# Kernel tuning notes

Measured on AMD Instinct MI355X. Metric: run time of the kernel, lower is better.

The kernel has to match this reference:

```python
import jax, jax.numpy as jnp
import numpy as np

HIDDEN = 256
HEADS = 8
HEAD_SIZE = HIDDEN // HEADS  # 32
CTX = 512
FF = 4 * HIDDEN
LN_EPS = 1e-5


def setup_inputs() -> dict:
    key = jax.random.key(0)
    ks = jax.random.split(key, 12)
    s = 0.02
    return {
        "x": jax.random.normal(ks[0], (32, CTX, HIDDEN), dtype=jnp.float32),
        # per-head Q/K/V projections, stored [H, D, E] ([in, out] orientation)
        "wq": jax.random.normal(ks[1], (HEADS, HIDDEN, HEAD_SIZE), dtype=jnp.float32) * s,
        "wk": jax.random.normal(ks[2], (HEADS, HIDDEN, HEAD_SIZE), dtype=jnp.float32) * s,
        "wv": jax.random.normal(ks[3], (HEADS, HIDDEN, HEAD_SIZE), dtype=jnp.float32) * s,
        "w_proj": jax.random.normal(ks[4], (HIDDEN, HIDDEN), dtype=jnp.float32) * s,
        "w1": jax.random.normal(ks[5], (HIDDEN, FF), dtype=jnp.float32) * s,
        "b1": jnp.zeros((FF,), dtype=jnp.float32),
        "w2": jax.random.normal(ks[6], (FF, HIDDEN), dtype=jnp.float32) * s,
        "b2": jnp.zeros((HIDDEN,), dtype=jnp.float32),
        "g_ln1": jnp.ones((HIDDEN,), dtype=jnp.float32),
        "be_ln1": jnp.zeros((HIDDEN,), dtype=jnp.float32),
        "g_ln2": jnp.ones((HIDDEN,), dtype=jnp.float32),
        "be_ln2": jnp.zeros((HIDDEN,), dtype=jnp.float32),
    }


def _layernorm(x, g, b):
    mu = jnp.mean(x, axis=-1, keepdims=True)
    var = jnp.var(x, axis=-1, keepdims=True)
    return (x - mu) * jax.lax.rsqrt(var + LN_EPS) * g + b


def reference(x, wq, wk, wv, w_proj, w1, b1, w2, b2, g_ln1, be_ln1, g_ln2, be_ln2):
    B, S, D = x.shape  # S == CTX
    # per-head projections: [B, H, S, E]
    q = jnp.einsum("bsd,hde->bhse", x, wq)
    k = jnp.einsum("bsd,hde->bhse", x, wk)
    v = jnp.einsum("bsd,hde->bhse", x, wv)
    scores = jnp.einsum("bhse,bhte->bhst", q, k) * (HEAD_SIZE ** -0.5)
    causal = jnp.tril(jnp.ones((S, S), dtype=bool))  # [S, S]
    scores = jnp.where(causal, scores, -jnp.inf)
    attn = jax.nn.softmax(scores, axis=-1)
    ctx = jnp.einsum("bhst,bhte->bhse", attn, v)
    ctx = ctx.transpose(0, 2, 1, 3).reshape(B, S, D)  # concat heads
    attn_out = ctx @ w_proj
    h = x + _layernorm(attn_out, g_ln1, be_ln1)
    ff = jax.nn.relu(h @ w1 + b1) @ w2 + b2
    return x + _layernorm(ff, g_ln2, be_ln2)
```

## Files before the change

kernel.cpp:

```cpp
#include <hip/hip_runtime.h>
#include <hip/hip_bf16.h>

#define B_   32
#define S_   512
#define D_   256
#define H_   8
#define E_   32
#define FF_  1024
#define T_   (B_ * S_)

typedef __attribute__((ext_vector_type(8))) short short8;
typedef __attribute__((ext_vector_type(4))) float f32x4;

static __device__ __forceinline__ unsigned short f2bf(float f) {
    union { float f; unsigned int u; } c; c.f = f;
    unsigned int u = c.u;
    u += 0x7fffu + ((u >> 16) & 1u);
    return (unsigned short)(u >> 16);
}
static __device__ __forceinline__ float bf2f(unsigned short u) {
    union { unsigned int u; float f; } c; c.u = ((unsigned int)u) << 16;
    return c.f;
}
static __device__ __forceinline__ unsigned int cvtpk(float lo, float hi) {
    unsigned int r;
    asm("v_cvt_pk_bf16_f32 %0, %1, %2" : "=v"(r) : "v"(lo), "v"(hi));
    return r;
}

#define GLOAD16(g, l) __builtin_amdgcn_global_load_lds( \
    (const __attribute__((address_space(1))) void*)(g), \
    (__attribute__((address_space(3))) void*)(l), 16, 0, 0)

__global__ void prep_kernel(const float* __restrict__ x,
                            const float* __restrict__ wq, const float* __restrict__ wk,
                            const float* __restrict__ wv, const float* __restrict__ w_proj,
                            const float* __restrict__ w1, const float* __restrict__ w2,
                            unsigned short* __restrict__ xb, unsigned short* __restrict__ Wqkv,
                            unsigned short* __restrict__ Wproj, unsigned short* __restrict__ W1t,
                            unsigned short* __restrict__ W2t) {
    int blk = blockIdx.x, tid = threadIdx.x;
    if (blk < 4096) {
        int i = blk * 256 + tid;
        float4 v = *(const float4*)&x[(size_t)i * 4];
        ushort4 o; o.x = f2bf(v.x); o.y = f2bf(v.y); o.z = f2bf(v.z); o.w = f2bf(v.w);
        *(ushort4*)&xb[(size_t)i * 4] = o;
    } else if (blk < 4864) {
        int idx = (blk - 4096) * 256 + tid;
        int nn = idx >> 8, k = idx & 255;
        int which = nn >> 8, r = nn & 255, h = r >> 5, e = r & 31;
        const float* w = (which == 0) ? wq : (which == 1 ? wk : wv);
        float v = w[(h * D_ + k) * E_ + e];
        if (which == 0) v *= 0.17677669529663687f * 1.4426950408889634f;
        Wqkv[idx] = f2bf(v);
    } else if (blk < 5120) {
        int idx = (blk - 4864) * 256 + tid;
        int nn = idx >> 8, k = idx & 255;
        Wproj[idx] = f2bf(w_proj[(size_t)k * 256 + nn]);
    } else if (blk < 6144) {
        int idx = (blk - 5120) * 256 + tid;
        int nn = idx >> 8, k = idx & 255;
        W1t[idx] = f2bf(w1[(size_t)k * 1024 + nn]);
    } else {
        int idx = (blk - 6144) * 256 + tid;
        int nn = idx >> 10, k = idx & 1023;
        W2t[idx] = f2bf(w2[(size_t)k * 256 + nn]);
    }
}

template <int EP, int BN>
__global__ __launch_bounds__(256) void gemm_mfma(const unsigned short* __restrict__ A,
                                                 const unsigned short* __restrict__ Bt,
                                                 const float* __restrict__ bias,
                                                 void* __restrict__ Cout,
                                                 unsigned short* __restrict__ Vout,
                                                 int M, int N, int K) {
    constexpr int FN = BN / 32;
    __shared__ char smem[16384 + BN * 128];
    const int tid = threadIdx.x;
    const int bm = blockIdx.y * 128, bn = blockIdx.x * BN;
    const int wave = tid >> 6, lane = tid & 63;
    const int l15 = lane & 15, kc = lane >> 4;
    const int wr = (wave >> 1) * 64, wc = (wave & 1) * (BN / 2);

    auto stage = [&](int buf, int kt) {
        int k0 = kt * 32;
        char* aBase = smem + buf * 8192;
        char* bBase = smem + 16384 + buf * (BN * 64);
        #pragma unroll
        for (int j = 0; j < 2; ++j) {
            int o = j * 256 + tid;
            int r = o >> 2, c = o & 3;
            int g = c ^ ((r >> 1) & 3);
            GLOAD16(A + (size_t)(bm + r) * K + k0 + g * 8, aBase + o * 16);
        }
        #pragma unroll
        for (int j = 0; j < BN / 64; ++j) {
            int o = j * 256 + tid;
            int r = o >> 2, c = o & 3;
            int g = c ^ ((r >> 1) & 3);
            GLOAD16(Bt + (size_t)(bn + r) * K + k0 + g * 8, bBase + o * 16);
        }
    };

    f32x4 acc[4][FN];
    #pragma unroll
    for (int m = 0; m < 4; ++m)
        #pragma unroll
        for (int n = 0; n < FN; ++n) acc[m][n] = (f32x4){0.f, 0.f, 0.f, 0.f};

    const int NT = K >> 5;
    stage(0, 0);
    __syncthreads();

    int buf = 0;
    for (int kt = 0; kt < NT; ++kt) {
        if (kt + 1 < NT) stage(buf ^ 1, kt + 1);
        const char* aBase = smem + buf * 8192;
        const char* bBase = smem + 16384 + buf * (BN * 64);
        short8 afr[4], bfr[FN];
        #pragma unroll
        for (int m = 0; m < 4; ++m) {
            int row = wr + m * 16 + l15;
            int cc = kc ^ ((row >> 1) & 3);
            afr[m] = *(const short8*)(aBase + row * 64 + cc * 16);
        }
        #pragma unroll
        for (int n = 0; n < FN; ++n) {
            int row = wc + n * 16 + l15;
            int cc = kc ^ ((row >> 1) & 3);
            bfr[n] = *(const short8*)(bBase + row * 64 + cc * 16);
        }
        #pragma unroll
        for (int m = 0; m < 4; ++m)
            #pragma unroll
            for (int n = 0; n < FN; ++n)
                acc[m][n] = __builtin_amdgcn_mfma_f32_16x16x32_bf16(afr[m], bfr[n], acc[m][n], 0, 0, 0);
        __syncthreads();
        buf ^= 1;
    }

    if (EP & 8) {
        #pragma unroll
        for (int n = 0; n < FN; ++n) {
            int col = bn + wc + n * 16 + l15;
            if (col < 512) {
                #pragma unroll
                for (int m = 0; m < 4; ++m) {
                    int row0 = bm + wr + m * 16 + kc * 4;
                    #pragma unroll
                    for (int j = 0; j < 4; ++j)
                        ((unsigned short*)Cout)[(size_t)(row0 + j) * 512 + col] = f2bf(acc[m][n][j]);
                }
            } else {
                int hh = (col - 512) >> 5, e = (col - 512) & 31;
                #pragma unroll
                for (int m = 0; m < 4; ++m) {
                    int row0 = bm + wr + m * 16 + kc * 4;
                    int bb = row0 >> 9, s0 = row0 & 511;
                    ushort4 o4;
                    o4.x = f2bf(acc[m][n][0]); o4.y = f2bf(acc[m][n][1]);
                    o4.z = f2bf(acc[m][n][2]); o4.w = f2bf(acc[m][n][3]);
                    *(ushort4*)&Vout[(size_t)(bb * 8 + hh) * 16384 + e * 512 + s0] = o4;
                }
            }
        }
    } else {
        #pragma unroll
        for (int n = 0; n < FN; ++n) {
            int col = bn + wc + n * 16 + l15;
            float bv = (EP & 1) ? bias[col] : 0.f;
            #pragma unroll
            for (int m = 0; m < 4; ++m) {
                int row0 = bm + wr + m * 16 + kc * 4;
                #pragma unroll
                for (int j = 0; j < 4; ++j) {
                    float v = acc[m][n][j] + bv;
                    if (EP & 2) v = fmaxf(v, 0.f);
                    if (EP & 4) ((unsigned short*)Cout)[(size_t)(row0 + j) * N + col] = f2bf(v);
                    else        ((float*)Cout)[(size_t)(row0 + j) * N + col] = v;
                }
            }
        }
    }
}

__global__ __launch_bounds__(256, 2) void attn_mfma(const unsigned short* __restrict__ qk,
                                                    const unsigned short* __restrict__ vtg,
                                                    unsigned short* __restrict__ ctx) {
    __shared__ unsigned short klds[512 * 32];
    __shared__ unsigned short vlds[32 * 512];
    __shared__ unsigned short plds[4][32 * 64];
    const int blk = blockIdx.x;
    const int bh = blk >> 1, qh = blk & 1;
    const int b = bh >> 3, h = bh & 7;
    const int tid = threadIdx.x;
    const int wave = tid >> 6, lane = tid & 63;
    const int l15 = lane & 15, kc = lane >> 4;

    const unsigned short* kg = qk + (size_t)b * 512 * 512 + 256 + h * 32;
    #pragma unroll
    for (int it = 0; it < 8; ++it) {
        int slot = it * 256 + tid;
        int r = slot >> 2, c = slot & 3;
        GLOAD16(kg + (size_t)r * 512 + (c ^ ((r >> 1) & 3)) * 8, (char*)klds + slot * 16);
    }
    #pragma unroll
    for (int it = 0; it < 8; ++it) {
        int slot = it * 256 + tid;
        int e = slot >> 6, c = slot & 63;
        GLOAD16(vtg + (size_t)bh * 16384 + e * 512 + (c ^ (e & 7)) * 8,
                (char*)vlds + slot * 16);
    }

    const int cA = qh * 4 + wave, cB = 15 - cA;
    short8 qfA[2], qfB[2];
    #pragma unroll
    for (int qm = 0; qm < 2; ++qm) {
        qfA[qm] = *(const short8*)(qk + (size_t)(b * 512 + cA * 32 + qm * 16 + l15) * 512 + h * 32 + kc * 8);
        qfB[qm] = *(const short8*)(qk + (size_t)(b * 512 + cB * 32 + qm * 16 + l15) * 512 + h * 32 + kc * 8);
    }
    __syncthreads();

    unsigned short* pw = plds[wave];
    const int xsw = (l15 & 7) << 1;

    auto process = [&](int cc_, const short8* qf) {
        const int nt = (cc_ >> 1) + 1;
        f32x4 Ofr[2][2];
        float mreg[2], lreg[2];
        #pragma unroll
        for (int qm = 0; qm < 2; ++qm) {
            Ofr[qm][0] = (f32x4){0.f, 0.f, 0.f, 0.f};
            Ofr[qm][1] = (f32x4){0.f, 0.f, 0.f, 0.f};
            mreg[qm] = -1e30f; lreg[qm] = 0.f;
        }
        for (int ti = 0; ti < nt; ++ti) {
            const int t0 = ti * 64;
            short8 kf[4];
            #pragma unroll
            for (int tn = 0; tn < 4; ++tn) {
                int row = t0 + tn * 16 + l15;
                int cx = kc ^ ((row >> 1) & 3);
                kf[tn] = *(const short8*)((const char*)klds + row * 64 + cx * 16);
            }
            const bool diag = (ti == nt - 1);

            #pragma unroll
            for (int qm = 0; qm < 2; ++qm) {
                f32x4 st[4];
                __builtin_amdgcn_s_setprio(1);
                #pragma unroll
                for (int tn = 0; tn < 4; ++tn)
                    st[tn] = __builtin_amdgcn_mfma_f32_16x16x32_bf16(kf[tn], qf[qm],
                                                                     (f32x4){0.f, 0.f, 0.f, 0.f}, 0, 0, 0);
                __builtin_amdgcn_s_setprio(0);
                if (diag) {
                    int qg = cc_ * 32 + qm * 16 + l15;
                    #pragma unroll
                    for (int tn = 0; tn < 4; ++tn)
                        #pragma unroll
                        for (int j = 0; j < 4; ++j)
                            if (t0 + tn * 16 + kc * 4 + j > qg) st[tn][j] = -1e30f;
                }
                float tmax = st[0][0];
                #pragma unroll
                for (int tn = 0; tn < 4; ++tn)
                    #pragma unroll
                    for (int j = 0; j < 4; ++j) tmax = fmaxf(tmax, st[tn][j]);
                tmax = fmaxf(tmax, __shfl_xor(tmax, 16));
                tmax = fmaxf(tmax, __shfl_xor(tmax, 32));

                if (__any(tmax > mreg[qm] + 11.5f)) {
                    float mn = fmaxf(mreg[qm], tmax);
                    float corr = __builtin_amdgcn_exp2f(mreg[qm] - mn);
                    lreg[qm] *= corr;
                    #pragma unroll
                    for (int j = 0; j < 4; ++j) {
                        float cj = __shfl(corr, kc * 4 + j, 16);
                        Ofr[qm][0][j] *= cj;
                        Ofr[qm][1][j] *= cj;
                    }
                    mreg[qm] = mn;
                }

                float psum = 0.f;
                #pragma unroll
                for (int tn = 0; tn < 4; ++tn) {
                    float p0 = __builtin_amdgcn_exp2f(st[tn][0] - mreg[qm]);
                    float p1 = __builtin_amdgcn_exp2f(st[tn][1] - mreg[qm]);
                    float p2 = __builtin_amdgcn_exp2f(st[tn][2] - mreg[qm]);
                    float p3 = __builtin_amdgcn_exp2f(st[tn][3] - mreg[qm]);
                    psum += (p0 + p1) + (p2 + p3);
                    uint2 w;
                    w.x = cvtpk(p0, p1);
                    w.y = cvtpk(p2, p3);
                    int tc = (tn * 4 + kc) ^ xsw;
                    *(uint2*)(pw + (qm * 16 + l15) * 64 + tc * 4) = w;
                }
                psum += __shfl_xor(psum, 16);
                psum += __shfl_xor(psum, 32);
                lreg[qm] += psum;
            }

            #pragma unroll
            for (int tt = 0; tt < 2; ++tt) {
                short8 pa[2];
                #pragma unroll
                for (int qm = 0; qm < 2; ++qm) {
                    int tcr = (tt * 8 + kc * 2) ^ xsw;
                    pa[qm] = *(const short8*)(pw + (qm * 16 + l15) * 64 + tcr * 4);
                }
                short8 vt[2];
                #pragma unroll
                for (int n = 0; n < 2; ++n) {
                    int e = n * 16 + l15;
                    int c = ((t0 >> 3) + tt * 4 + kc) ^ (e & 7);
                    vt[n] = *(const short8*)(vlds + e * 512 + c * 8);
                }
                __builtin_amdgcn_s_setprio(1);
                #pragma unroll
                for (int qm = 0; qm < 2; ++qm)
                    #pragma unroll
                    for (int n = 0; n < 2; ++n)
                        Ofr[qm][n] = __builtin_amdgcn_mfma_f32_16x16x32_bf16(pa[qm], vt[n], Ofr[qm][n], 0, 0, 0);
                __builtin_amdgcn_s_setprio(0);
            }
        }

        #pragma unroll
        for (int qm = 0; qm < 2; ++qm) {
            float linv = 1.f / lreg[qm];
            #pragma unroll
            for (int j = 0; j < 4; ++j) {
                float lj = __shfl(linv, kc * 4 + j, 16);
                size_t base = (size_t)(b * 512 + cc_ * 32 + qm * 16 + kc * 4 + j) * 256 + h * 32;
                ctx[base + l15]      = f2bf(Ofr[qm][0][j] * lj);
                ctx[base + 16 + l15] = f2bf(Ofr[qm][1][j] * lj);
            }
        }
    };

    process(cA, qfA);
    process(cB, qfB);
}

template <int OUTF32>
__global__ __launch_bounds__(256) void ln_residual(const unsigned short* __restrict__ in,
                                                   const float* __restrict__ x,
                                                   const float* __restrict__ g,
                                                   const float* __restrict__ be,
                                                   void* __restrict__ out) {
    int token = blockIdx.x * 4 + (threadIdx.x >> 6);
    int lane = threadIdx.x & 63;
    ushort4 iv = *(const ushort4*)&in[(size_t)token * D_ + lane * 4];
    float4 v;
    v.x = bf2f(iv.x); v.y = bf2f(iv.y); v.z = bf2f(iv.z); v.w = bf2f(iv.w);
    float s  = v.x + v.y + v.z + v.w;
    float s2 = v.x * v.x + v.y * v.y + v.z * v.z + v.w * v.w;
    #pragma unroll
    for (int off = 1; off < 64; off <<= 1) {
        s  += __shfl_xor(s, off);
        s2 += __shfl_xor(s2, off);
    }
    float mu  = s * (1.f / D_);
    float var = s2 * (1.f / D_) - mu * mu;
    float r   = rsqrtf(var + 1e-5f);
    float4 xv = *(const float4*)&x[(size_t)token * D_ + lane * 4];
    float4 gv = *(const float4*)&g[lane * 4];
    float4 bv = *(const float4*)&be[lane * 4];
    float4 o;
    o.x = xv.x + (v.x - mu) * r * gv.x + bv.x;
    o.y = xv.y + (v.y - mu) * r * gv.y + bv.y;
    o.z = xv.z + (v.z - mu) * r * gv.z + bv.z;
    o.w = xv.w + (v.w - mu) * r * gv.w + bv.w;
    if (OUTF32) {
        *(float4*)((float*)out + (size_t)token * D_ + lane * 4) = o;
    } else {
        ushort4 o4; o4.x = f2bf(o.x); o4.y = f2bf(o.y); o4.z = f2bf(o.z); o4.w = f2bf(o.w);
        *(ushort4*)((unsigned short*)out + (size_t)token * D_ + lane * 4) = o4;
    }
}

extern "C" void kernel_launch(void* const* d_in, const int* in_sizes, int n_in,
                              void* d_out, int out_size, void* d_ws, size_t ws_size,
                              hipStream_t stream) {
    (void)in_sizes; (void)n_in; (void)out_size; (void)ws_size;
    const float* x      = (const float*)d_in[0];
    const float* wq     = (const float*)d_in[1];
    const float* wk     = (const float*)d_in[2];
    const float* wv     = (const float*)d_in[3];
    const float* w_proj = (const float*)d_in[4];
    const float* w1     = (const float*)d_in[5];
    const float* b1     = (const float*)d_in[6];
    const float* w2     = (const float*)d_in[7];
    const float* b2     = (const float*)d_in[8];
    const float* g1     = (const float*)d_in[9];
    const float* be1    = (const float*)d_in[10];
    const float* g2     = (const float*)d_in[11];
    const float* be2    = (const float*)d_in[12];
    float* out = (float*)d_out;

    char* W = (char*)d_ws;
    unsigned short* qk      = (unsigned short*)(W + 0);
    unsigned short* vtg     = (unsigned short*)(W + 16777216);
    unsigned short* xb      = (unsigned short*)(W + 25165824);
    unsigned short* ctx     = (unsigned short*)(W + 25165824);
    unsigned short* attnout = (unsigned short*)(W + 33554432);
    unsigned short* hbuf    = (unsigned short*)(W + 41943040);
    unsigned short* ffout   = (unsigned short*)(W + 50331648);
    unsigned short* ff1     = (unsigned short*)(W + 0);
    unsigned short* Wqkv_t  = (unsigned short*)(W + 58720256);
    unsigned short* Wproj_t = (unsigned short*)(W + 59113472);
    unsigned short* W1_t    = (unsigned short*)(W + 59244544);
    unsigned short* W2_t    = (unsigned short*)(W + 59768832);

    prep_kernel<<<7168, 256, 0, stream>>>(x, wq, wk, wv, w_proj, w1, w2,
                                          xb, Wqkv_t, Wproj_t, W1_t, W2_t);

    gemm_mfma<8, 128><<<dim3(6, T_ / 128), 256, 0, stream>>>(xb, Wqkv_t, nullptr, qk, vtg, T_, 768, 256);

    attn_mfma<<<B_ * H_ * 2, 256, 0, stream>>>(qk, vtg, ctx);

    gemm_mfma<4, 64><<<dim3(4, T_ / 128), 256, 0, stream>>>(ctx, Wproj_t, nullptr, attnout, nullptr, T_, 256, 256);

    ln_residual<0><<<T_ / 4, 256, 0, stream>>>(attnout, x, g1, be1, hbuf);

    gemm_mfma<7, 128><<<dim3(8, T_ / 128), 256, 0, stream>>>(hbuf, W1_t, b1, ff1, nullptr, T_, FF_, 256);

    gemm_mfma<5, 64><<<dim3(4, T_ / 128), 256, 0, stream>>>(ff1, W2_t, b2, ffout, nullptr, T_, 256, 1024);

    ln_residual<1><<<T_ / 4, 256, 0, stream>>>(ffout, x, g2, be2, out);
}
```

Before: 119.3 us.

## Fuse LayerNorm-residual epilogue into output-projection and FF2 GEMMs

Adds a GEMM kernel whose blocks each cover 64 full rows of the 256-wide output. The LayerNorm statistics are reduced in registers and shared memory and the residual is added in the epilogue. This replaces the two GEMM + ln_residual pairs, removing the bf16 round-trip of the intermediate outputs and two launches. Blocks now span the full N, so there are fewer and larger blocks (256 per launch), which lowers parallelism and adds register pressure from the 2x8 accumulator tiles.

```diff
diff --git a/kernel.cpp b/kernel.cpp
--- a/kernel.cpp
+++ b/kernel.cpp
@@ -185,6 +185,135 @@
     }
 }
 
+template <int BIAS, int OUTF32>
+__global__ __launch_bounds__(256) void gemm_ln2(const unsigned short* __restrict__ A,
+                                                const unsigned short* __restrict__ Bt,
+                                                const float* __restrict__ bias,
+                                                const float* __restrict__ xres,
+                                                const float* __restrict__ gw,
+                                                const float* __restrict__ bw,
+                                                void* __restrict__ Cout,
+                                                int K) {
+    __shared__ char smem[40960];
+    __shared__ float sred[2][2][64];
+    const int tid = threadIdx.x;
+    const int bm = blockIdx.x * 64;
+    const int wave = tid >> 6, lane = tid & 63;
+    const int l15 = lane & 15, kc = lane >> 4;
+    const int wr = (wave >> 1) * 32, wc = (wave & 1) * 128;
+
+    auto stage = [&](int buf, int kt) {
+        int k0 = kt * 32;
+        char* aBase = smem + buf * 4096;
+        char* bBase = smem + 8192 + buf * 16384;
+        {
+            int o = tid;
+            int r = o >> 2, c = o & 3;
+            int g = c ^ ((r >> 1) & 3);
+            GLOAD16(A + (size_t)(bm + r) * K + k0 + g * 8, aBase + o * 16);
+        }
+        #pragma unroll
+        for (int j = 0; j < 4; ++j) {
+            int o = j * 256 + tid;
+            int r = o >> 2, c = o & 3;
+            int g = c ^ ((r >> 1) & 3);
+            GLOAD16(Bt + (size_t)r * K + k0 + g * 8, bBase + o * 16);
+        }
+    };
+
+    f32x4 acc[2][8];
+    #pragma unroll
+    for (int m = 0; m < 2; ++m)
+        #pragma unroll
+        for (int n = 0; n < 8; ++n) acc[m][n] = (f32x4){0.f, 0.f, 0.f, 0.f};
+
+    const int NT = K >> 5;
+    stage(0, 0);
+    __syncthreads();
+
+    int buf = 0;
+    for (int kt = 0; kt < NT; ++kt) {
+        if (kt + 1 < NT) stage(buf ^ 1, kt + 1);
+        const char* aBase = smem + buf * 4096;
+        const char* bBase = smem + 8192 + buf * 16384;
+        short8 afr[2], bfr[8];
+        #pragma unroll
+        for (int m = 0; m < 2; ++m) {
+            int row = wr + m * 16 + l15;
+            int cc = kc ^ ((row >> 1) & 3);
+            afr[m] = *(const short8*)(aBase + row * 64 + cc * 16);
+        }
+        #pragma unroll
+        for (int n = 0; n < 8; ++n) {
+            int row = wc + n * 16 + l15;
+            int cc = kc ^ ((row >> 1) & 3);
+            bfr[n] = *(const short8*)(bBase + row * 64 + cc * 16);
+        }
+        #pragma unroll
+        for (int m = 0; m < 2; ++m)
+            #pragma unroll
+            for (int n = 0; n < 8; ++n)
+                acc[m][n] = __builtin_amdgcn_mfma_f32_16x16x32_bf16(afr[m], bfr[n], acc[m][n], 0, 0, 0);
+        __syncthreads();
+        buf ^= 1;
+    }
+
+    float gv[8], bev[8];
+    #pragma unroll
+    for (int n = 0; n < 8; ++n) {
+        int col = wc + n * 16 + l15;
+        gv[n] = gw[col]; bev[n] = bw[col];
+        if (BIAS) {
+            float bb = bias[col];
+            #pragma unroll
+            for (int m = 0; m < 2; ++m)
+                #pragma unroll
+                for (int j = 0; j < 4; ++j) acc[m][n][j] += bb;
+        }
+    }
+
+    #pragma unroll
+    for (int m = 0; m < 2; ++m) {
+        #pragma unroll
+        for (int j = 0; j < 4; ++j) {
+            float s = 0.f, s2 = 0.f;
+            #pragma unroll
+            for (int n = 0; n < 8; ++n) { float v = acc[m][n][j]; s += v; s2 += v * v; }
+            #pragma unroll
+            for (int off = 1; off < 16; off <<= 1) {
+                s += __shfl_xor(s, off); s2 += __shfl_xor(s2, off);
+            }
+            if (l15 == 0) {
+                int rl = wr + m * 16 + kc * 4 + j;
+                sred[wave & 1][0][rl] = s;
+                sred[wave & 1][1][rl] = s2;
+            }
+        }
+    }
+    __syncthreads();
+
+    #pragma unroll
+    for (int m = 0; m < 2; ++m) {
+        #pragma unroll
+        for (int j = 0; j < 4; ++j) {
+            int rl = wr + m * 16 + kc * 4 + j;
+            float stot  = sred[0][0][rl] + sred[1][0][rl];
+            float s2tot = sred[0][1][rl] + sred[1][1][rl];
+            float mu  = stot * (1.f / 256.f);
+            float var = s2tot * (1.f / 256.f) - mu * mu;
+            float rr  = rsqrtf(var + 1e-5f);
+            int rowg = bm + rl;
+            #pragma unroll
+            for (int n = 0; n < 8; ++n) {
+                int col = wc + n * 16 + l15;
+                float o = xres[(size_t)rowg * 256 + col] + (acc[m][n][j] - mu) * rr * gv[n] + bev[n];
+                if (OUTF32) ((float*)Cout)[(size_t)rowg * 256 + col] = o;
+                else ((unsigned short*)Cout)[(size_t)rowg * 256 + col] = f2bf(o);
+            }
+        }
+    }
+}
+
 __global__ __launch_bounds__(256, 2) void attn_mfma(const unsigned short* __restrict__ qk,
                                                     const unsigned short* __restrict__ vtg,
                                                     unsigned short* __restrict__ ctx) {
@@ -343,43 +472,6 @@
 
     process(cA, qfA);
     process(cB, qfB);
-}
-
-template <int OUTF32>
-__global__ __launch_bounds__(256) void ln_residual(const unsigned short* __restrict__ in,
-                                                   const float* __restrict__ x,
-                                                   const float* __restrict__ g,
-                                                   const float* __restrict__ be,
-                                                   void* __restrict__ out) {
-    int token = blockIdx.x * 4 + (threadIdx.x >> 6);
-    int lane = threadIdx.x & 63;
-    ushort4 iv = *(const ushort4*)&in[(size_t)token * D_ + lane * 4];
-    float4 v;
-    v.x = bf2f(iv.x); v.y = bf2f(iv.y); v.z = bf2f(iv.z); v.w = bf2f(iv.w);
-    float s  = v.x + v.y + v.z + v.w;
-    float s2 = v.x * v.x + v.y * v.y + v.z * v.z + v.w * v.w;
-    #pragma unroll
-    for (int off = 1; off < 64; off <<= 1) {
-        s  += __shfl_xor(s, off);
-        s2 += __shfl_xor(s2, off);
-    }
-    float mu  = s * (1.f / D_);
-    float var = s2 * (1.f / D_) - mu * mu;
-    float r   = rsqrtf(var + 1e-5f);
-    float4 xv = *(const float4*)&x[(size_t)token * D_ + lane * 4];
-    float4 gv = *(const float4*)&g[lane * 4];
-    float4 bv = *(const float4*)&be[lane * 4];
-    float4 o;
-    o.x = xv.x + (v.x - mu) * r * gv.x + bv.x;
-    o.y = xv.y + (v.y - mu) * r * gv.y + bv.y;
-    o.z = xv.z + (v.z - mu) * r * gv.z + bv.z;
-    o.w = xv.w + (v.w - mu) * r * gv.w + bv.w;
-    if (OUTF32) {
-        *(float4*)((float*)out + (size_t)token * D_ + lane * 4) = o;
-    } else {
-        ushort4 o4; o4.x = f2bf(o.x); o4.y = f2bf(o.y); o4.z = f2bf(o.z); o4.w = f2bf(o.w);
-        *(ushort4*)((unsigned short*)out + (size_t)token * D_ + lane * 4) = o4;
-    }
 }
 
 extern "C" void kernel_launch(void* const* d_in, const int* in_sizes, int n_in,
@@ -406,14 +498,12 @@
     unsigned short* vtg     = (unsigned short*)(W + 16777216);
     unsigned short* xb      = (unsigned short*)(W + 25165824);
     unsigned short* ctx     = (unsigned short*)(W + 25165824);
-    unsigned short* attnout = (unsigned short*)(W + 33554432);
-    unsigned short* hbuf    = (unsigned short*)(W + 41943040);
-    unsigned short* ffout   = (unsigned short*)(W + 50331648);
+    unsigned short* hbuf    = (unsigned short*)(W + 33554432);
     unsigned short* ff1     = (unsigned short*)(W + 0);
-    unsigned short* Wqkv_t  = (unsigned short*)(W + 58720256);
-    unsigned short* Wproj_t = (unsigned short*)(W + 59113472);
-    unsigned short* W1_t    = (unsigned short*)(W + 59244544);
-    unsigned short* W2_t    = (unsigned short*)(W + 59768832);
+    unsigned short* Wqkv_t  = (unsigned short*)(W + 50331648);
+    unsigned short* Wproj_t = (unsigned short*)(W + 50724864);
+    unsigned short* W1_t    = (unsigned short*)(W + 50855936);
+    unsigned short* W2_t    = (unsigned short*)(W + 51380224);
 
     prep_kernel<<<7168, 256, 0, stream>>>(x, wq, wk, wv, w_proj, w1, w2,
                                           xb, Wqkv_t, Wproj_t, W1_t, W2_t);
@@ -422,13 +512,9 @@
 
     attn_mfma<<<B_ * H_ * 2, 256, 0, stream>>>(qk, vtg, ctx);
 
-    gemm_mfma<4, 64><<<dim3(4, T_ / 128), 256, 0, stream>>>(ctx, Wproj_t, nullptr, attnout, nullptr, T_, 256, 256);
-
-    ln_residual<0><<<T_ / 4, 256, 0, stream>>>(attnout, x, g1, be1, hbuf);
+    gemm_ln2<0, 0><<<T_ / 64, 256, 0, stream>>>(ctx, Wproj_t, nullptr, x, g1, be1, hbuf, 256);
 
     gemm_mfma<7, 128><<<dim3(8, T_ / 128), 256, 0, stream>>>(hbuf, W1_t, b1, ff1, nullptr, T_, FF_, 256);
 
-    gemm_mfma<5, 64><<<dim3(4, T_ / 128), 256, 0, stream>>>(ff1, W2_t, b2, ffout, nullptr, T_, 256, 1024);
-
-    ln_residual<1><<<T_ / 4, 256, 0, stream>>>(ffout, x, g2, be2, out);
-}
+    gemm_ln2<1, 1><<<T_ / 64, 256, 0, stream>>>(ff1, W2_t, b2, x, g2, be2, out, 1024);
+}
```

Result: no change. 119.2 us (-0.0%).
